# Optimization experiments

Measured on AMD Instinct MI355X. Metric: run time of the kernel, lower is better.

Reference implementation:

```python
import jax, jax.numpy as jnp
import numpy as np

BIG = 1e30  # finite 'inf' so masked-min keeps clean gradients

def setup_inputs() -> dict:
    key = jax.random.key(0)
    k1, k2, k3, k4 = jax.random.split(key, 4)
    B, N, C = 8, 2048, 3
    pred = jax.random.normal(k1, (B, N, C), dtype=jnp.float32)
    target = jax.random.normal(k2, (B, N, C), dtype=jnp.float32)
    points = jax.random.normal(k3, (B, N, C), dtype=jnp.float32)
    mask = jax.random.randint(k4, (B, N), 0, 2, dtype=jnp.int32)
    return {"pred": pred, "target": target, "mask": mask, "points": points}

def _loss(pred, target, points, maskf):
    # masked L1 term: per-point mean over xyz, masked mean over valid points
    l1_map = jnp.mean(jnp.abs(pred - target), axis=2) * maskf      # [B,N]
    l1 = l1_map.sum() / maskf.sum()

    clean = points + target                                        # [B,N,3]
    predp = points + pred                                          # [B,N,3]
    # pairwise L1 distances between clean (rows) and pred (cols)
    D = jnp.sum(jnp.abs(clean[:, :, None, :] - predp[:, None, :, :]), axis=-1)  # [B,N,N]

    valid_cnt = maskf.sum(axis=1)                                  # [B]
    # clean -> nearest valid pred point (mask columns j)
    min_x = jnp.min(jnp.where(maskf[:, None, :] > 0, D, BIG), axis=2)  # [B,N]
    # pred -> nearest valid clean point (mask rows i)
    min_y = jnp.min(jnp.where(maskf[:, :, None] > 0, D, BIG), axis=1)  # [B,N]
    cham = (min_x * maskf).sum(axis=1) / valid_cnt \
         + (min_y * maskf).sum(axis=1) / valid_cnt                 # [B]
    cd = cham.mean()  # per-batch chamfer summed then divided by B

    # converging_to == 'chamfer'
    return l1 + jnp.exp(-l1) * cd

def reference(pred, target, mask, points):
    maskf = mask.astype(pred.dtype)
    return _loss(pred, target, points, maskf)
```

## Files before the change

### kernel.cpp

```cpp
#include <hip/hip_runtime.h>
#include <math.h>
#include <float.h>

#define BB 8
#define NN 2048
#define BN (BB * NN)
#define BLK 256
#define Q 4
#define QSPLIT 2
#define CSPLIT 32
#define CCHUNK (NN / CSPLIT)

#define MINPART_FLOATS (CSPLIT * 2 * BN)

__global__ __launch_bounds__(BLK) void k_main(const float* __restrict__ pred,
                                              const float* __restrict__ target,
                                              const float* __restrict__ points,
                                              const int* __restrict__ mask,
                                              float* __restrict__ minpart,
                                              float* __restrict__ l1part,
                                              float* __restrict__ cntpart) {
    int bid = blockIdx.x;
    int cs = bid & (CSPLIT - 1);
    int qs = (bid >> 5) & (QSPLIT - 1);
    int b = (bid >> 6) & 7;
    int task = bid >> 9;
    int t = threadIdx.x;

    const float* dq = task ? pred : target;
    const float* dc = task ? target : pred;

    __shared__ float4 cand[CCHUNK];
    if (t < CCHUNK) {
        int g = b * NN + cs * CCHUNK + t;
        size_t g3 = (size_t)g * 3;
        float x, y, z;
        if (mask[g]) {
            x = points[g3 + 0] + dc[g3 + 0];
            y = points[g3 + 1] + dc[g3 + 1];
            z = points[g3 + 2] + dc[g3 + 2];
        } else {
            x = y = z = 1e30f;
        }
        cand[t] = make_float4(x, y, z, 0.f);
    }
    __syncthreads();

    float qx[Q], qy[Q], qz[Q], mn[Q];
    #pragma unroll
    for (int q = 0; q < Q; ++q) {
        int qi = qs * (BLK * Q) + q * BLK + t;
        size_t g3 = (size_t)(b * NN + qi) * 3;
        qx[q] = points[g3 + 0] + dq[g3 + 0];
        qy[q] = points[g3 + 1] + dq[g3 + 1];
        qz[q] = points[g3 + 2] + dq[g3 + 2];
        mn[q] = FLT_MAX;
    }

    #pragma unroll 4
    for (int j = 0; j < CCHUNK; ++j) {
        float4 c = cand[j];
        #pragma unroll
        for (int q = 0; q < Q; ++q) {
            float d = fabsf(qx[q] - c.x) + fabsf(qy[q] - c.y) + fabsf(qz[q] - c.z);
            mn[q] = fminf(mn[q], d);
        }
    }

    float* mp = minpart + (size_t)cs * (2 * BN) + (size_t)task * BN + b * NN;
    #pragma unroll
    for (int q = 0; q < Q; ++q)
        mp[qs * (BLK * Q) + q * BLK + t] = mn[q];

    if (task == 0 && cs == 0) {
        float s = 0.f, c = 0.f;
        #pragma unroll
        for (int q = 0; q < Q; ++q) {
            int gi = b * NN + qs * (BLK * Q) + q * BLK + t;
            size_t g3 = (size_t)gi * 3;
            float m = (float)mask[gi];
            s += (fabsf(pred[g3 + 0] - target[g3 + 0]) +
                  fabsf(pred[g3 + 1] - target[g3 + 1]) +
                  fabsf(pred[g3 + 2] - target[g3 + 2])) * (1.0f / 3.0f) * m;
            c += m;
        }
        for (int off = 32; off; off >>= 1) {
            s += __shfl_down(s, off, 64);
            c += __shfl_down(c, off, 64);
        }
        __shared__ float ls[4], lc[4];
        if ((t & 63) == 0) { ls[t >> 6] = s; lc[t >> 6] = c; }
        __syncthreads();
        if (t == 0) {
            l1part[b * QSPLIT + qs]  = ls[0] + ls[1] + ls[2] + ls[3];
            cntpart[b * QSPLIT + qs] = lc[0] + lc[1] + lc[2] + lc[3];
        }
    }
}

__global__ __launch_bounds__(BLK) void k_reduce(const float* __restrict__ minpart,
                                                const int* __restrict__ mask,
                                                float* __restrict__ champart) {
    int tb = blockIdx.x;
    int qs = tb & 3;
    int b = (tb >> 2) & 7;
    int task = tb >> 5;
    int t = threadIdx.x;

    float v = 0.f;
    #pragma unroll
    for (int k = 0; k < 2; ++k) {
        int qi = qs * 512 + k * BLK + t;
        size_t idx = (size_t)task * BN + b * NN + qi;
        float mn = minpart[idx];
        #pragma unroll
        for (int cs = 1; cs < CSPLIT; ++cs)
            mn = fminf(mn, minpart[(size_t)cs * (2 * BN) + idx]);
        v += mn * (float)mask[b * NN + qi];
    }
    for (int off = 32; off; off >>= 1) v += __shfl_down(v, off, 64);
    __shared__ float ls[4];
    if ((t & 63) == 0) ls[t >> 6] = v;
    __syncthreads();
    if (t == 0) champart[tb] = ls[0] + ls[1] + ls[2] + ls[3];
}

__global__ void k_fin(const float* __restrict__ champart,
                      const float* __restrict__ l1part,
                      const float* __restrict__ cntpart,
                      float* __restrict__ out) {
    if (threadIdx.x == 0) {
        double cnt[BB], msum = 0.0, l1num = 0.0;
        for (int b = 0; b < BB; ++b) {
            cnt[b] = (double)cntpart[2 * b] + (double)cntpart[2 * b + 1];
            msum += cnt[b];
            l1num += (double)l1part[2 * b] + (double)l1part[2 * b + 1];
        }
        double l1 = l1num / msum;
        double cd = 0.0;
        for (int b = 0; b < BB; ++b) {
            double ch = 0.0;
            for (int qs = 0; qs < 4; ++qs)
                ch += (double)champart[(b << 2) + qs] + (double)champart[32 + (b << 2) + qs];
            cd += ch / cnt[b];
        }
        cd *= (1.0 / BB);
        out[0] = (float)(l1 + exp(-l1) * cd);
    }
}

extern "C" void kernel_launch(void* const* d_in, const int* in_sizes, int n_in,
                              void* d_out, int out_size, void* d_ws, size_t ws_size,
                              hipStream_t stream) {
    const float* pred   = (const float*)d_in[0];
    const float* target = (const float*)d_in[1];
    const int*   mask   = (const int*)d_in[2];
    const float* points = (const float*)d_in[3];
    float* out = (float*)d_out;

    float* minpart  = (float*)d_ws;
    float* champart = (float*)((char*)d_ws + (size_t)MINPART_FLOATS * 4);
    float* l1part   = champart + 64;
    float* cntpart  = l1part + 16;

    k_main<<<2 * 8 * QSPLIT * CSPLIT, BLK, 0, stream>>>(pred, target, points, mask,
                                                        minpart, l1part, cntpart);
    k_reduce<<<64, BLK, 0, stream>>>(minpart, mask, champart);
    k_fin<<<1, 64, 0, stream>>>(champart, l1part, cntpart, out);
}
```

Baseline: 21.85 us.

## Retile main kernel to full query rows per block and fuse final reduction via last-block counter

Each block of the main kernel now handles all 2048 queries of a batch, eight per thread, against a 32-candidate chunk, with 64 candidate splits instead of two query splits times 32 candidate splits. The inner loop consumes two candidates per iteration. The L1 partial sums are spread over 8 blocks per batch. The final scalar computation is folded into the reduce kernel through an atomic ticket counter, so the last block computes the output and one kernel launch is dropped. The cost is a larger minpart buffer for the reduce to scan (64 partials per point instead of 32) and more registers per thread.

```diff
diff --git a/kernel.cpp b/kernel.cpp
--- a/kernel.cpp
+++ b/kernel.cpp
@@ -6,9 +6,8 @@
 #define NN 2048
 #define BN (BB * NN)
 #define BLK 256
-#define Q 4
-#define QSPLIT 2
-#define CSPLIT 32
+#define Q 8
+#define CSPLIT 64
 #define CCHUNK (NN / CSPLIT)
 
 #define MINPART_FLOATS (CSPLIT * 2 * BN)
@@ -19,13 +18,15 @@
                                               const int* __restrict__ mask,
                                               float* __restrict__ minpart,
                                               float* __restrict__ l1part,
-                                              float* __restrict__ cntpart) {
+                                              float* __restrict__ cntpart,
+                                              unsigned int* __restrict__ counter) {
     int bid = blockIdx.x;
     int cs = bid & (CSPLIT - 1);
-    int qs = (bid >> 5) & (QSPLIT - 1);
     int b = (bid >> 6) & 7;
     int task = bid >> 9;
     int t = threadIdx.x;
+
+    if (bid == 0 && t == 0) *counter = 0u;
 
     const float* dq = task ? pred : target;
     const float* dc = task ? target : pred;
@@ -34,13 +35,11 @@
     if (t < CCHUNK) {
         int g = b * NN + cs * CCHUNK + t;
         size_t g3 = (size_t)g * 3;
-        float x, y, z;
+        float x = 1e30f, y = 1e30f, z = 1e30f;
         if (mask[g]) {
             x = points[g3 + 0] + dc[g3 + 0];
             y = points[g3 + 1] + dc[g3 + 1];
             z = points[g3 + 2] + dc[g3 + 2];
-        } else {
-            x = y = z = 1e30f;
         }
         cand[t] = make_float4(x, y, z, 0.f);
     }
@@ -49,8 +48,7 @@
     float qx[Q], qy[Q], qz[Q], mn[Q];
     #pragma unroll
     for (int q = 0; q < Q; ++q) {
-        int qi = qs * (BLK * Q) + q * BLK + t;
-        size_t g3 = (size_t)(b * NN + qi) * 3;
+        size_t g3 = (size_t)(b * NN + q * BLK + t) * 3;
         qx[q] = points[g3 + 0] + dq[g3 + 0];
         qy[q] = points[g3 + 1] + dq[g3 + 1];
         qz[q] = points[g3 + 2] + dq[g3 + 2];
@@ -58,32 +56,30 @@
     }
 
     #pragma unroll 4
-    for (int j = 0; j < CCHUNK; ++j) {
-        float4 c = cand[j];
+    for (int j = 0; j < CCHUNK; j += 2) {
+        float4 c0 = cand[j];
+        float4 c1 = cand[j + 1];
         #pragma unroll
         for (int q = 0; q < Q; ++q) {
-            float d = fabsf(qx[q] - c.x) + fabsf(qy[q] - c.y) + fabsf(qz[q] - c.z);
-            mn[q] = fminf(mn[q], d);
+            float d0 = fabsf(qx[q] - c0.x) + fabsf(qy[q] - c0.y) + fabsf(qz[q] - c0.z);
+            float d1 = fabsf(qx[q] - c1.x) + fabsf(qy[q] - c1.y) + fabsf(qz[q] - c1.z);
+            mn[q] = fminf(fminf(d0, d1), mn[q]);
         }
     }
 
     float* mp = minpart + (size_t)cs * (2 * BN) + (size_t)task * BN + b * NN;
     #pragma unroll
     for (int q = 0; q < Q; ++q)
-        mp[qs * (BLK * Q) + q * BLK + t] = mn[q];
+        mp[q * BLK + t] = mn[q];
 
-    if (task == 0 && cs == 0) {
-        float s = 0.f, c = 0.f;
-        #pragma unroll
-        for (int q = 0; q < Q; ++q) {
-            int gi = b * NN + qs * (BLK * Q) + q * BLK + t;
-            size_t g3 = (size_t)gi * 3;
-            float m = (float)mask[gi];
-            s += (fabsf(pred[g3 + 0] - target[g3 + 0]) +
-                  fabsf(pred[g3 + 1] - target[g3 + 1]) +
-                  fabsf(pred[g3 + 2] - target[g3 + 2])) * (1.0f / 3.0f) * m;
-            c += m;
-        }
+    if (task == 0 && cs < 8) {
+        int gi = b * NN + cs * BLK + t;
+        size_t g3 = (size_t)gi * 3;
+        float m = (float)mask[gi];
+        float s = (fabsf(pred[g3 + 0] - target[g3 + 0]) +
+                   fabsf(pred[g3 + 1] - target[g3 + 1]) +
+                   fabsf(pred[g3 + 2] - target[g3 + 2])) * (1.0f / 3.0f) * m;
+        float c = m;
         for (int off = 32; off; off >>= 1) {
             s += __shfl_down(s, off, 64);
             c += __shfl_down(c, off, 64);
@@ -92,17 +88,21 @@
         if ((t & 63) == 0) { ls[t >> 6] = s; lc[t >> 6] = c; }
         __syncthreads();
         if (t == 0) {
-            l1part[b * QSPLIT + qs]  = ls[0] + ls[1] + ls[2] + ls[3];
-            cntpart[b * QSPLIT + qs] = lc[0] + lc[1] + lc[2] + lc[3];
+            l1part[b * 8 + cs]  = ls[0] + ls[1] + ls[2] + ls[3];
+            cntpart[b * 8 + cs] = lc[0] + lc[1] + lc[2] + lc[3];
         }
     }
 }
 
-__global__ __launch_bounds__(BLK) void k_reduce(const float* __restrict__ minpart,
+__global__ __launch_bounds__(BLK) void k_redfin(const float* __restrict__ minpart,
                                                 const int* __restrict__ mask,
-                                                float* __restrict__ champart) {
+                                                const float* __restrict__ l1part,
+                                                const float* __restrict__ cntpart,
+                                                float* __restrict__ champart,
+                                                unsigned int* __restrict__ counter,
+                                                float* __restrict__ out) {
     int tb = blockIdx.x;
-    int qs = tb & 3;
+    int s4 = tb & 3;
     int b = (tb >> 2) & 7;
     int task = tb >> 5;
     int t = threadIdx.x;
@@ -110,7 +110,7 @@
     float v = 0.f;
     #pragma unroll
     for (int k = 0; k < 2; ++k) {
-        int qi = qs * 512 + k * BLK + t;
+        int qi = s4 * 512 + k * BLK + t;
         size_t idx = (size_t)task * BN + b * NN + qi;
         float mn = minpart[idx];
         #pragma unroll
@@ -119,30 +119,42 @@
         v += mn * (float)mask[b * NN + qi];
     }
     for (int off = 32; off; off >>= 1) v += __shfl_down(v, off, 64);
+
     __shared__ float ls[4];
+    __shared__ int isLast;
+    __shared__ float ch[64];
     if ((t & 63) == 0) ls[t >> 6] = v;
     __syncthreads();
-    if (t == 0) champart[tb] = ls[0] + ls[1] + ls[2] + ls[3];
-}
+    if (t == 0) {
+        float bs = ls[0] + ls[1] + ls[2] + ls[3];
+        __hip_atomic_store(&champart[tb], bs, __ATOMIC_RELEASE, __HIP_MEMORY_SCOPE_AGENT);
+        int ticket = __hip_atomic_fetch_add(counter, 1u, __ATOMIC_ACQ_REL, __HIP_MEMORY_SCOPE_AGENT);
+        isLast = (ticket == 63);
+    }
+    __syncthreads();
+    if (!isLast) return;
 
-__global__ void k_fin(const float* __restrict__ champart,
-                      const float* __restrict__ l1part,
-                      const float* __restrict__ cntpart,
-                      float* __restrict__ out) {
-    if (threadIdx.x == 0) {
+    if (t < 64) ch[t] = __hip_atomic_load(&champart[t], __ATOMIC_ACQUIRE, __HIP_MEMORY_SCOPE_AGENT);
+    __syncthreads();
+    if (t == 0) {
         double cnt[BB], msum = 0.0, l1num = 0.0;
-        for (int b = 0; b < BB; ++b) {
-            cnt[b] = (double)cntpart[2 * b] + (double)cntpart[2 * b + 1];
-            msum += cnt[b];
-            l1num += (double)l1part[2 * b] + (double)l1part[2 * b + 1];
+        for (int b2 = 0; b2 < BB; ++b2) {
+            double cb = 0.0;
+            for (int k = 0; k < 8; ++k) {
+                cb += (double)cntpart[b2 * 8 + k];
+                l1num += (double)l1part[b2 * 8 + k];
+            }
+            cnt[b2] = cb;
+            msum += cb;
         }
         double l1 = l1num / msum;
         double cd = 0.0;
-        for (int b = 0; b < BB; ++b) {
-            double ch = 0.0;
-            for (int qs = 0; qs < 4; ++qs)
-                ch += (double)champart[(b << 2) + qs] + (double)champart[32 + (b << 2) + qs];
-            cd += ch / cnt[b];
+        for (int b2 = 0; b2 < BB; ++b2) {
+            double chb = 0.0;
+            for (int tk = 0; tk < 2; ++tk)
+                for (int s = 0; s < 4; ++s)
+                    chb += (double)ch[tk * 32 + b2 * 4 + s];
+            cd += chb / cnt[b2];
         }
         cd *= (1.0 / BB);
         out[0] = (float)(l1 + exp(-l1) * cd);
@@ -159,12 +171,14 @@
     float* out = (float*)d_out;
 
     float* minpart  = (float*)d_ws;
-    float* champart = (float*)((char*)d_ws + (size_t)MINPART_FLOATS * 4);
-    float* l1part   = champart + 64;
-    float* cntpart  = l1part + 16;
+    char* tail = (char*)d_ws + (size_t)MINPART_FLOATS * 4;
+    float* champart = (float*)tail;
+    float* l1part   = (float*)(tail + 256);
+    float* cntpart  = (float*)(tail + 512);
+    unsigned int* counter = (unsigned int*)(tail + 768);
 
-    k_main<<<2 * 8 * QSPLIT * CSPLIT, BLK, 0, stream>>>(pred, target, points, mask,
-                                                        minpart, l1part, cntpart);
-    k_reduce<<<64, BLK, 0, stream>>>(minpart, mask, champart);
-    k_fin<<<1, 64, 0, stream>>>(champart, l1part, cntpart, out);
+    k_main<<<2 * BB * CSPLIT, BLK, 0, stream>>>(pred, target, points, mask,
+                                                minpart, l1part, cntpart, counter);
+    k_redfin<<<64, BLK, 0, stream>>>(minpart, mask, l1part, cntpart,
+                                     champart, counter, out);
 }
```

Result: slower. 26.52 us (+21.4%).
